# Kernel optimization log

Hardware: AMD Instinct MI355X
Metric: run time of the kernel (lower is better)

The kernel has to match this reference:

```python
import jax, jax.numpy as jnp
import numpy as np

N_NODES = 100000
N_EDGES = 1600000
DIM = 128
N_SEEDS = 15000


def _gcn_stack(edges, x, Ws):
    """Multi-layer GCN with sym-normalized edge-list aggregation, residual, ReLU.
    edges: [2, E] int; x: [N, d] float; Ws: list of [d, d] weights."""
    n = x.shape[0]
    loop = jnp.arange(n, dtype=edges.dtype)
    src = jnp.concatenate([edges[0], loop])  # add self-loops
    dst = jnp.concatenate([edges[1], loop])
    deg = jax.ops.segment_sum(jnp.ones(src.shape, x.dtype), dst, num_segments=n)
    dinv = jax.lax.rsqrt(deg)  # deg >= 1 thanks to self-loops
    norm = dinv[src] * dinv[dst]  # [E+N]
    for W in Ws:
        h = x @ W                                   # [N, d] dense transform
        msg = norm[:, None] * h[src]                # gather + scale, [E+N, d]
        agg = jax.ops.segment_sum(msg, dst, num_segments=n)  # scatter-add
        x = jax.nn.relu(agg + h)                    # residual + activation
    return x


def setup_inputs() -> dict:
    key = jax.random.key(0)
    ks = jax.random.split(key, 8)
    scale = 1.0 / np.sqrt(DIM)
    return {
        "sr_ent_seeds": jax.random.randint(ks[0], (N_SEEDS,), 0, N_NODES),
        "tg_ent_seeds": jax.random.randint(ks[1], (N_SEEDS,), 0, N_NODES),
        "edges_sr": jax.random.randint(ks[2], (2, N_EDGES), 0, N_NODES),
        "edges_tg": jax.random.randint(ks[3], (2, N_EDGES), 0, N_NODES),
        "embedding_sr": jax.random.normal(ks[4], (N_NODES, DIM), jnp.float32),
        "embedding_tg": jax.random.normal(ks[5], (N_NODES, DIM), jnp.float32),
        "W0": jax.random.normal(ks[6], (DIM, DIM), jnp.float32) * scale,
        "W1": jax.random.normal(ks[7], (DIM, DIM), jnp.float32) * scale,
    }


def reference(sr_ent_seeds, tg_ent_seeds, edges_sr, edges_tg,
              embedding_sr, embedding_tg, W0, W1):
    Ws = [W0, W1]
    sr_ent_hid = _gcn_stack(edges_sr, embedding_sr, Ws)
    tg_ent_hid = _gcn_stack(edges_tg, embedding_tg, Ws)
    sr_seed_hid = sr_ent_hid[sr_ent_seeds]
    tg_seed_hid = tg_ent_hid[tg_ent_seeds]
    return (sr_seed_hid, tg_seed_hid, sr_ent_hid, tg_ent_hid)
```

## Files before the change

kernel.cpp:

```cpp
#include <hip/hip_runtime.h>

#define NN 100000
#define NE 1600000
#define NT (2 * NN)
#define ET (2 * NE)
#define DIM 128
#define NS 15000
#define SB2 ((NT + 255) / 256)
#define PAD 136
#define NRANGE 16
#define RSZ (NT / NRANGE)
#define CH 16
#define BCAP 210000
#define NE4 (NE / 4)

typedef __attribute__((ext_vector_type(8))) short frag_ab;
typedef __attribute__((ext_vector_type(4))) float frag_cd;
typedef __attribute__((ext_vector_type(4))) int i4;

__device__ __forceinline__ unsigned short f2bf(float f) {
    unsigned int u = __float_as_uint(f);
    u += 0x7fff + ((u >> 16) & 1);
    return (unsigned short)(u >> 16);
}
__device__ __forceinline__ float bflo(unsigned int u) { return __uint_as_float(u << 16); }
__device__ __forceinline__ float bfhi(unsigned int u) { return __uint_as_float(u & 0xffff0000u); }

__global__ __launch_bounds__(256) void bucket_k(const int* __restrict__ e_sr,
                                                const int* __restrict__ e_tg,
                                                int* __restrict__ gcur,
                                                int* __restrict__ bkt) {
    __shared__ int bcnt[4][NRANGE];
    __shared__ int bbase[4][NRANGE];
    const int tid = threadIdx.x;
    if (tid < 4 * NRANGE) ((int*)bcnt)[tid] = 0;
    __syncthreads();
    const int g = blockIdx.x * 256 + tid;
    i4 s4, d4;
    if (g < NE4) {
        s4 = *((const i4*)e_sr + g);
        d4 = *((const i4*)e_sr + NE4 + g);
    } else {
        s4 = *((const i4*)e_tg + g - NE4);
        d4 = *((const i4*)e_tg + g);
        s4 += NN;
        d4 += NN;
    }
    const int wv = tid >> 6;
    int rr[4], lr[4];
#pragma unroll
    for (int j = 0; j < 4; ++j) {
        rr[j] = d4[j] / RSZ;
        lr[j] = atomicAdd(&bcnt[wv][rr[j]], 1);
    }
    __syncthreads();
    if (tid < NRANGE) {
        const int t0 = bcnt[0][tid], t1 = bcnt[1][tid];
        const int t2 = bcnt[2][tid], t3 = bcnt[3][tid];
        const int b = atomicAdd(&gcur[tid], t0 + t1 + t2 + t3);
        bbase[0][tid] = b;
        bbase[1][tid] = b + t0;
        bbase[2][tid] = b + t0 + t1;
        bbase[3][tid] = b + t0 + t1 + t2;
    }
    __syncthreads();
#pragma unroll
    for (int j = 0; j < 4; ++j) {
        const int dtl = d4[j] - rr[j] * RSZ;
        bkt[bbase[wv][rr[j]] + lr[j]] = (dtl << 18) | s4[j];
    }
}

__global__ __launch_bounds__(1024) void hist_k(const int* __restrict__ gcur,
                                               const int* __restrict__ bkt,
                                               int* __restrict__ P) {
    __shared__ int lc[RSZ];
    const int r = blockIdx.x & (NRANGE - 1);
    const int c = blockIdx.x >> 4;
    const int lo = r * RSZ;
    for (int i = threadIdx.x; i < RSZ; i += 1024) lc[i] = 0;
    __syncthreads();
    const int n_r = gcur[r] - r * BCAP;
    const int S = (n_r + CH - 1) / CH;
    const int s0 = c * S;
    int s1 = s0 + S; if (s1 > n_r) s1 = n_r;
    for (int v = s0 + threadIdx.x; v < s1; v += 1024) {
        const unsigned int w = (unsigned int)bkt[r * BCAP + v];
        atomicAdd(&lc[w >> 18], 1);
    }
    __syncthreads();
    for (int i = threadIdx.x; i < RSZ; i += 1024) P[c * NT + lo + i] = lc[i];
}

__global__ __launch_bounds__(256) void reduceA_k(const int* __restrict__ P,
                                                 int* __restrict__ cnt,
                                                 float* __restrict__ dinv,
                                                 int* __restrict__ bsum) {
    __shared__ int sh[256];
    const int t = threadIdx.x;
    const int i = blockIdx.x * 256 + t;
    int s = 0;
    if (i < NT) {
#pragma unroll
        for (int c = 0; c < CH; ++c) s += P[c * NT + i];
        cnt[i] = s;
        dinv[i] = rsqrtf((float)(s + 1));
    }
    sh[t] = s;
    __syncthreads();
    for (int off = 128; off > 0; off >>= 1) {
        if (t < off) sh[t] += sh[t + off];
        __syncthreads();
    }
    if (t == 0) bsum[blockIdx.x] = sh[0];
}

__global__ __launch_bounds__(1024) void scanB_k(int* bsum, int* row_ptr) {
    __shared__ int s[1024];
    const int t = threadIdx.x;
    const int v = (t < SB2) ? bsum[t] : 0;
    s[t] = v;
    __syncthreads();
    for (int off = 1; off < 1024; off <<= 1) {
        int add = (t >= off) ? s[t - off] : 0;
        __syncthreads();
        s[t] += add;
        __syncthreads();
    }
    if (t < SB2) bsum[t] = s[t] - v;
    if (t == SB2 - 1) row_ptr[NT] = s[t];
}

__global__ __launch_bounds__(256) void scanCbase_k(const int* __restrict__ cnt,
                                                   const int* __restrict__ bsum,
                                                   int* __restrict__ row_ptr,
                                                   int* __restrict__ P) {
    __shared__ int s[256];
    const int t = threadIdx.x;
    const int i = blockIdx.x * 256 + t;
    const int v = (i < NT) ? cnt[i] : 0;
    s[t] = v;
    __syncthreads();
    for (int off = 1; off < 256; off <<= 1) {
        int add = (t >= off) ? s[t - off] : 0;
        __syncthreads();
        s[t] += add;
        __syncthreads();
    }
    if (i < NT) {
        const int rp = bsum[blockIdx.x] + s[t] - v;
        row_ptr[i] = rp;
        int run = rp;
#pragma unroll
        for (int c = 0; c < CH; ++c) {
            const int pv = P[c * NT + i];
            P[c * NT + i] = run;
            run += pv;
        }
    }
}

__global__ __launch_bounds__(1024) void fillp_k(const int* __restrict__ gcur,
                                                const int* __restrict__ bkt,
                                                const int* __restrict__ P,
                                                int* __restrict__ csr_src) {
    __shared__ int cur[RSZ];
    const int r = blockIdx.x & (NRANGE - 1);
    const int c = blockIdx.x >> 4;
    const int lo = r * RSZ;
    for (int i = threadIdx.x; i < RSZ; i += 1024) cur[i] = P[c * NT + lo + i];
    __syncthreads();
    const int n_r = gcur[r] - r * BCAP;
    const int S = (n_r + CH - 1) / CH;
    const int s0 = c * S;
    int s1 = s0 + S; if (s1 > n_r) s1 = n_r;
    for (int v = s0 + threadIdx.x; v < s1; v += 1024) {
        const unsigned int w = (unsigned int)bkt[r * BCAP + v];
        const int pos = atomicAdd(&cur[w >> 18], 1);
        csr_src[pos] = (int)(w & 0x3FFFFu);
    }
}

__global__ __launch_bounds__(256) void convW2_k(const float* __restrict__ W0,
                                                const float* __restrict__ W1,
                                                unsigned short* __restrict__ wt0,
                                                unsigned short* __restrict__ wt1,
                                                int* __restrict__ gcur) {
    int i = blockIdx.x * 256 + threadIdx.x;
    if (blockIdx.x == 0 && threadIdx.x < NRANGE) gcur[threadIdx.x] = threadIdx.x * BCAP;
    if (i >= 2 * DIM * DIM) return;
    const float* W = (i < DIM * DIM) ? W0 : W1;
    unsigned short* wt = (i < DIM * DIM) ? wt0 : wt1;
    const int ii = i & (DIM * DIM - 1);
    const int n = ii & 127, k = ii >> 7;
    wt[n * DIM + k] = f2bf(W[k * DIM + n]);
}

__global__ __launch_bounds__(256) void gemmE_k(const float* __restrict__ emb_sr,
                                               const float* __restrict__ emb_tg,
                                               const unsigned short* __restrict__ Wt,
                                               const float* __restrict__ dinv,
                                               unsigned short* __restrict__ Gb) {
    __shared__ unsigned short xs[64 * PAD];
    __shared__ unsigned short ws[128 * PAD];
    const int tid = threadIdx.x;
    const int row0 = blockIdx.x * 64;

    for (int i = tid; i < 128 * 16; i += 256) {
        const int r = i >> 4, o = i & 15;
        *(uint4*)&ws[r * PAD + o * 8] = *(const uint4*)&Wt[r * DIM + o * 8];
    }
    for (int i = tid; i < 64 * 32; i += 256) {
        const int r = i >> 5, o = i & 31;
        const int gr = row0 + r;
        const float4 v = (gr < NN) ? ((const float4*)emb_sr)[gr * 32 + o]
                                   : ((const float4*)emb_tg)[(gr - NN) * 32 + o];
        ushort4 b;
        b.x = f2bf(v.x); b.y = f2bf(v.y); b.z = f2bf(v.z); b.w = f2bf(v.w);
        *(ushort4*)&xs[r * PAD + o * 4] = b;
    }
    __syncthreads();

    const int wave = tid >> 6;
    const int lane = tid & 63;
    const int m = lane & 15;
    const int quad = lane >> 4;
    const int rbase = wave * 16;

    frag_cd acc[8];
#pragma unroll
    for (int ct = 0; ct < 8; ct++) acc[ct] = (frag_cd){0.f, 0.f, 0.f, 0.f};

#pragma unroll
    for (int ks = 0; ks < 4; ks++) {
        const frag_ab a = *(const frag_ab*)&xs[(rbase + m) * PAD + ks * 32 + quad * 8];
#pragma unroll
        for (int ct = 0; ct < 8; ct++) {
            const frag_ab b = *(const frag_ab*)&ws[(ct * 16 + m) * PAD + ks * 32 + quad * 8];
            acc[ct] = __builtin_amdgcn_mfma_f32_16x16x32_bf16(a, b, acc[ct], 0, 0, 0);
        }
    }

#pragma unroll
    for (int r = 0; r < 4; r++) {
        const int grow = row0 + rbase + quad * 4 + r;
        const float dv = dinv[grow];
#pragma unroll
        for (int ct = 0; ct < 8; ct++)
            Gb[grow * DIM + ct * 16 + m] = f2bf(dv * acc[ct][r]);
    }
}

__global__ __launch_bounds__(256) void gemm_mfma_k(const unsigned short* __restrict__ Xb,
                                                   const unsigned short* __restrict__ Wt,
                                                   const float* __restrict__ dinv,
                                                   unsigned short* __restrict__ Gb) {
    __shared__ unsigned short xs[64 * PAD];
    __shared__ unsigned short ws[128 * PAD];
    const int tid = threadIdx.x;
    const int row0 = blockIdx.x * 64;

    for (int i = tid; i < 128 * 16; i += 256) {
        const int r = i >> 4, o = i & 15;
        *(uint4*)&ws[r * PAD + o * 8] = *(const uint4*)&Wt[r * DIM + o * 8];
    }
    for (int i = tid; i < 64 * 16; i += 256) {
        const int r = i >> 4, o = i & 15;
        *(uint4*)&xs[r * PAD + o * 8] = *(const uint4*)&Xb[(row0 + r) * DIM + o * 8];
    }
    __syncthreads();

    const int wave = tid >> 6;
    const int lane = tid & 63;
    const int m = lane & 15;
    const int quad = lane >> 4;
    const int rbase = wave * 16;

    frag_cd acc[8];
#pragma unroll
    for (int ct = 0; ct < 8; ct++) acc[ct] = (frag_cd){0.f, 0.f, 0.f, 0.f};

#pragma unroll
    for (int ks = 0; ks < 4; ks++) {
        const frag_ab a = *(const frag_ab*)&xs[(rbase + m) * PAD + ks * 32 + quad * 8];
#pragma unroll
        for (int ct = 0; ct < 8; ct++) {
            const frag_ab b = *(const frag_ab*)&ws[(ct * 16 + m) * PAD + ks * 32 + quad * 8];
            acc[ct] = __builtin_amdgcn_mfma_f32_16x16x32_bf16(a, b, acc[ct], 0, 0, 0);
        }
    }

#pragma unroll
    for (int r = 0; r < 4; r++) {
        const int grow = row0 + rbase + quad * 4 + r;
        const float dv = dinv[grow];
#pragma unroll
        for (int ct = 0; ct < 8; ct++)
            Gb[grow * DIM + ct * 16 + m] = f2bf(dv * acc[ct][r]);
    }
}

template <bool OUT_BF16>
__global__ __launch_bounds__(256) void pull_k(const int* __restrict__ row_ptr,
                                              const int* __restrict__ csr_src,
                                              const float* __restrict__ dinv,
                                              const unsigned short* __restrict__ Gb,
                                              float* __restrict__ outf,
                                              unsigned short* __restrict__ outb) {
    const int node = (blockIdx.x * 256 + threadIdx.x) >> 6;
    if (node >= NT) return;
    const int lane = threadIdx.x & 63;
    const unsigned int* __restrict__ G2 = (const unsigned int*)Gb;

    const int beg = row_ptr[node];
    const int end = row_ptr[node + 1];
    const float d = dinv[node];
    const float sq = 1.0f / d;

    const unsigned int gu = G2[node * 64 + lane];
    float sx = bflo(gu);
    float sy = bfhi(gu);
    const float hx = sx * sq;
    const float hy = sy * sq;

    for (int base = beg; base < end; base += 64) {
        int rem = end - base; if (rem > 64) rem = 64;
        const int sl = (lane < rem) ? csr_src[base + lane] : 0;
        int j = 0;
        for (; j + 16 <= rem; j += 16) {
            int ss[16];
            unsigned int mm[16];
#pragma unroll
            for (int q = 0; q < 16; ++q) ss[q] = __shfl(sl, j + q);
#pragma unroll
            for (int q = 0; q < 16; ++q) mm[q] = G2[ss[q] * 64 + lane];
#pragma unroll
            for (int q = 0; q < 16; ++q) { sx += bflo(mm[q]); sy += bfhi(mm[q]); }
        }
        for (; j + 8 <= rem; j += 8) {
            int ss[8];
            unsigned int mm[8];
#pragma unroll
            for (int q = 0; q < 8; ++q) ss[q] = __shfl(sl, j + q);
#pragma unroll
            for (int q = 0; q < 8; ++q) mm[q] = G2[ss[q] * 64 + lane];
#pragma unroll
            for (int q = 0; q < 8; ++q) { sx += bflo(mm[q]); sy += bfhi(mm[q]); }
        }
        for (; j + 4 <= rem; j += 4) {
            int ss[4];
            unsigned int mm[4];
#pragma unroll
            for (int q = 0; q < 4; ++q) ss[q] = __shfl(sl, j + q);
#pragma unroll
            for (int q = 0; q < 4; ++q) mm[q] = G2[ss[q] * 64 + lane];
#pragma unroll
            for (int q = 0; q < 4; ++q) { sx += bflo(mm[q]); sy += bfhi(mm[q]); }
        }
        for (; j < rem; ++j) {
            const int s = __shfl(sl, j);
            const unsigned int mu = G2[s * 64 + lane];
            sx += bflo(mu);
            sy += bfhi(mu);
        }
    }
    const float ax = fmaxf(d * sx + hx, 0.f);
    const float ay = fmaxf(d * sy + hy, 0.f);
    if (OUT_BF16) {
        ((unsigned int*)outb)[node * 64 + lane] =
            (unsigned int)f2bf(ax) | ((unsigned int)f2bf(ay) << 16);
    } else {
        float2 o; o.x = ax; o.y = ay;
        ((float2*)outf)[node * 64 + lane] = o;
    }
}

__global__ __launch_bounds__(256) void gather2_k(const int* __restrict__ sr_seeds,
                                                 const int* __restrict__ tg_seeds,
                                                 const float* __restrict__ ent,
                                                 float* __restrict__ sr_out,
                                                 float* __restrict__ tg_out) {
    const int gid = blockIdx.x * 256 + threadIdx.x;
    const int s = gid >> 5;
    if (s >= 2 * NS) return;
    const int q = gid & 31;
    const bool tg = s >= NS;
    const int si = tg ? s - NS : s;
    const int node = tg ? tg_seeds[si] + NN : sr_seeds[si];
    float* o = tg ? tg_out : sr_out;
    ((float4*)o)[si * 32 + q] = ((const float4*)ent)[node * 32 + q];
}

extern "C" void kernel_launch(void* const* d_in, const int* in_sizes, int n_in,
                              void* d_out, int out_size, void* d_ws, size_t ws_size,
                              hipStream_t stream) {
    const int* sr_seeds = (const int*)d_in[0];
    const int* tg_seeds = (const int*)d_in[1];
    const int* edges_sr = (const int*)d_in[2];
    const int* edges_tg = (const int*)d_in[3];
    const float* emb_sr = (const float*)d_in[4];
    const float* emb_tg = (const float*)d_in[5];
    const float* W0 = (const float*)d_in[6];
    const float* W1 = (const float*)d_in[7];
    float* out = (float*)d_out;

    int* cnt = (int*)d_ws;
    float* dinv = (float*)(cnt + 200704);
    int* row_ptr = (int*)(dinv + 200704);
    int* bsum = row_ptr + 200704;
    int* csr_src = bsum + 1024;
    unsigned short* wt0 = (unsigned short*)(csr_src + ET);
    unsigned short* wt1 = wt0 + DIM * DIM;
    unsigned short* hb = wt1 + DIM * DIM;
    int* P = (int*)hb;
    int* bkt = P + CH * NT;
    int* gcur = bsum + 800;

    float* sr_seed_out = out;
    float* tg_seed_out = out + (long long)NS * DIM;
    float* ent = out + (long long)2 * NS * DIM;
    unsigned short* xb = (unsigned short*)ent;

    const int gGemm = (NT + 63) / 64;
    const int gPull = NT / 4;
    const int gBkt = ET / 1024;
    const int gHF = NRANGE * CH;

    convW2_k<<<(2 * DIM * DIM + 255) / 256, 256, 0, stream>>>(W0, W1, wt0, wt1, gcur);

    bucket_k<<<gBkt, 256, 0, stream>>>(edges_sr, edges_tg, gcur, bkt);
    hist_k<<<gHF, 1024, 0, stream>>>(gcur, bkt, P);
    reduceA_k<<<SB2, 256, 0, stream>>>(P, cnt, dinv, bsum);
    scanB_k<<<1, 1024, 0, stream>>>(bsum, row_ptr);
    scanCbase_k<<<SB2, 256, 0, stream>>>(cnt, bsum, row_ptr, P);
    fillp_k<<<gHF, 1024, 0, stream>>>(gcur, bkt, P, csr_src);

    gemmE_k<<<gGemm, 256, 0, stream>>>(emb_sr, emb_tg, wt0, dinv, hb);
    pull_k<true><<<gPull, 256, 0, stream>>>(row_ptr, csr_src, dinv, hb, nullptr, xb);
    gemm_mfma_k<<<gGemm, 256, 0, stream>>>(xb, wt1, dinv, hb);
    pull_k<false><<<gPull, 256, 0, stream>>>(row_ptr, csr_src, dinv, hb, ent, nullptr);

    const int gSeed = (2 * NS * 32 + 255) / 256;
    gather2_k<<<gSeed, 256, 0, stream>>>(sr_seeds, tg_seeds, ent, sr_seed_out, tg_seed_out);
}
```

Measured before the change: 564.5 us.

## Split pull wave into half-waves, fuse block scan, read weights from global

The pull kernel now splits each 64-lane wave into two half-waves. Each lane loads 8-byte uint2 chunks, so two neighbour rows are gathered at once, and the halves are combined with a cross-lane xor shuffle. The single-block scanB kernel is removed: each scanCbase block reduces its preceding block sums itself, and the total is hardcoded to ET. The GEMM kernels stop staging weights in LDS and read B fragments directly from global memory. This cuts a launch and LDS traffic, at the cost of redundant prefix reads and uncached weight loads per block.

```diff
diff --git a/kernel.cpp b/kernel.cpp
--- a/kernel.cpp
+++ b/kernel.cpp
@@ -115,22 +115,6 @@
     if (t == 0) bsum[blockIdx.x] = sh[0];
 }
 
-__global__ __launch_bounds__(1024) void scanB_k(int* bsum, int* row_ptr) {
-    __shared__ int s[1024];
-    const int t = threadIdx.x;
-    const int v = (t < SB2) ? bsum[t] : 0;
-    s[t] = v;
-    __syncthreads();
-    for (int off = 1; off < 1024; off <<= 1) {
-        int add = (t >= off) ? s[t - off] : 0;
-        __syncthreads();
-        s[t] += add;
-        __syncthreads();
-    }
-    if (t < SB2) bsum[t] = s[t] - v;
-    if (t == SB2 - 1) row_ptr[NT] = s[t];
-}
-
 __global__ __launch_bounds__(256) void scanCbase_k(const int* __restrict__ cnt,
                                                    const int* __restrict__ bsum,
                                                    int* __restrict__ row_ptr,
@@ -138,6 +122,16 @@
     __shared__ int s[256];
     const int t = threadIdx.x;
     const int i = blockIdx.x * 256 + t;
+    int acc = 0;
+    for (int b = t; b < blockIdx.x; b += 256) acc += bsum[b];
+    s[t] = acc;
+    __syncthreads();
+    for (int off = 128; off > 0; off >>= 1) {
+        if (t < off) s[t] += s[t + off];
+        __syncthreads();
+    }
+    const int boff = s[0];
+    __syncthreads();
     const int v = (i < NT) ? cnt[i] : 0;
     s[t] = v;
     __syncthreads();
@@ -147,8 +141,9 @@
         s[t] += add;
         __syncthreads();
     }
+    if (blockIdx.x == 0 && t == 0) row_ptr[NT] = ET;
     if (i < NT) {
-        const int rp = bsum[blockIdx.x] + s[t] - v;
+        const int rp = boff + s[t] - v;
         row_ptr[i] = rp;
         int run = rp;
 #pragma unroll
@@ -202,14 +197,9 @@
                                                const float* __restrict__ dinv,
                                                unsigned short* __restrict__ Gb) {
     __shared__ unsigned short xs[64 * PAD];
-    __shared__ unsigned short ws[128 * PAD];
     const int tid = threadIdx.x;
     const int row0 = blockIdx.x * 64;
 
-    for (int i = tid; i < 128 * 16; i += 256) {
-        const int r = i >> 4, o = i & 15;
-        *(uint4*)&ws[r * PAD + o * 8] = *(const uint4*)&Wt[r * DIM + o * 8];
-    }
     for (int i = tid; i < 64 * 32; i += 256) {
         const int r = i >> 5, o = i & 31;
         const int gr = row0 + r;
@@ -236,7 +226,7 @@
         const frag_ab a = *(const frag_ab*)&xs[(rbase + m) * PAD + ks * 32 + quad * 8];
 #pragma unroll
         for (int ct = 0; ct < 8; ct++) {
-            const frag_ab b = *(const frag_ab*)&ws[(ct * 16 + m) * PAD + ks * 32 + quad * 8];
+            const frag_ab b = *(const frag_ab*)&Wt[(ct * 16 + m) * DIM + ks * 32 + quad * 8];
             acc[ct] = __builtin_amdgcn_mfma_f32_16x16x32_bf16(a, b, acc[ct], 0, 0, 0);
         }
     }
@@ -256,14 +246,9 @@
                                                    const float* __restrict__ dinv,
                                                    unsigned short* __restrict__ Gb) {
     __shared__ unsigned short xs[64 * PAD];
-    __shared__ unsigned short ws[128 * PAD];
     const int tid = threadIdx.x;
     const int row0 = blockIdx.x * 64;
 
-    for (int i = tid; i < 128 * 16; i += 256) {
-        const int r = i >> 4, o = i & 15;
-        *(uint4*)&ws[r * PAD + o * 8] = *(const uint4*)&Wt[r * DIM + o * 8];
-    }
     for (int i = tid; i < 64 * 16; i += 256) {
         const int r = i >> 4, o = i & 15;
         *(uint4*)&xs[r * PAD + o * 8] = *(const uint4*)&Xb[(row0 + r) * DIM + o * 8];
@@ -285,7 +270,7 @@
         const frag_ab a = *(const frag_ab*)&xs[(rbase + m) * PAD + ks * 32 + quad * 8];
 #pragma unroll
         for (int ct = 0; ct < 8; ct++) {
-            const frag_ab b = *(const frag_ab*)&ws[(ct * 16 + m) * PAD + ks * 32 + quad * 8];
+            const frag_ab b = *(const frag_ab*)&Wt[(ct * 16 + m) * DIM + ks * 32 + quad * 8];
             acc[ct] = __builtin_amdgcn_mfma_f32_16x16x32_bf16(a, b, acc[ct], 0, 0, 0);
         }
     }
@@ -310,68 +295,81 @@
     const int node = (blockIdx.x * 256 + threadIdx.x) >> 6;
     if (node >= NT) return;
     const int lane = threadIdx.x & 63;
-    const unsigned int* __restrict__ G2 = (const unsigned int*)Gb;
+    const int half = lane >> 5;
+    const int col = lane & 31;
+    const uint2* __restrict__ G4 = (const uint2*)Gb;
 
     const int beg = row_ptr[node];
     const int end = row_ptr[node + 1];
     const float d = dinv[node];
     const float sq = 1.0f / d;
 
-    const unsigned int gu = G2[node * 64 + lane];
-    float sx = bflo(gu);
-    float sy = bfhi(gu);
-    const float hx = sx * sq;
-    const float hy = sy * sq;
+    const uint2 su = G4[node * 32 + col];
+    float a0, a1, a2, a3;
+    if (half == 0) {
+        a0 = bflo(su.x); a1 = bfhi(su.x); a2 = bflo(su.y); a3 = bfhi(su.y);
+    } else {
+        a0 = a1 = a2 = a3 = 0.f;
+    }
 
     for (int base = beg; base < end; base += 64) {
         int rem = end - base; if (rem > 64) rem = 64;
         const int sl = (lane < rem) ? csr_src[base + lane] : 0;
         int j = 0;
         for (; j + 16 <= rem; j += 16) {
-            int ss[16];
-            unsigned int mm[16];
-#pragma unroll
-            for (int q = 0; q < 16; ++q) ss[q] = __shfl(sl, j + q);
-#pragma unroll
-            for (int q = 0; q < 16; ++q) mm[q] = G2[ss[q] * 64 + lane];
-#pragma unroll
-            for (int q = 0; q < 16; ++q) { sx += bflo(mm[q]); sy += bfhi(mm[q]); }
+            int ss[8]; uint2 mm[8];
+#pragma unroll
+            for (int q = 0; q < 8; ++q) ss[q] = __shfl(sl, j + 2 * q + half);
+#pragma unroll
+            for (int q = 0; q < 8; ++q) mm[q] = G4[ss[q] * 32 + col];
+#pragma unroll
+            for (int q = 0; q < 8; ++q) {
+                a0 += bflo(mm[q].x); a1 += bfhi(mm[q].x);
+                a2 += bflo(mm[q].y); a3 += bfhi(mm[q].y);
+            }
         }
         for (; j + 8 <= rem; j += 8) {
-            int ss[8];
-            unsigned int mm[8];
-#pragma unroll
-            for (int q = 0; q < 8; ++q) ss[q] = __shfl(sl, j + q);
-#pragma unroll
-            for (int q = 0; q < 8; ++q) mm[q] = G2[ss[q] * 64 + lane];
-#pragma unroll
-            for (int q = 0; q < 8; ++q) { sx += bflo(mm[q]); sy += bfhi(mm[q]); }
-        }
-        for (; j + 4 <= rem; j += 4) {
-            int ss[4];
-            unsigned int mm[4];
-#pragma unroll
-            for (int q = 0; q < 4; ++q) ss[q] = __shfl(sl, j + q);
-#pragma unroll
-            for (int q = 0; q < 4; ++q) mm[q] = G2[ss[q] * 64 + lane];
-#pragma unroll
-            for (int q = 0; q < 4; ++q) { sx += bflo(mm[q]); sy += bfhi(mm[q]); }
-        }
-        for (; j < rem; ++j) {
-            const int s = __shfl(sl, j);
-            const unsigned int mu = G2[s * 64 + lane];
-            sx += bflo(mu);
-            sy += bfhi(mu);
-        }
-    }
-    const float ax = fmaxf(d * sx + hx, 0.f);
-    const float ay = fmaxf(d * sy + hy, 0.f);
-    if (OUT_BF16) {
-        ((unsigned int*)outb)[node * 64 + lane] =
-            (unsigned int)f2bf(ax) | ((unsigned int)f2bf(ay) << 16);
-    } else {
-        float2 o; o.x = ax; o.y = ay;
-        ((float2*)outf)[node * 64 + lane] = o;
+            int ss[4]; uint2 mm[4];
+#pragma unroll
+            for (int q = 0; q < 4; ++q) ss[q] = __shfl(sl, j + 2 * q + half);
+#pragma unroll
+            for (int q = 0; q < 4; ++q) mm[q] = G4[ss[q] * 32 + col];
+#pragma unroll
+            for (int q = 0; q < 4; ++q) {
+                a0 += bflo(mm[q].x); a1 += bfhi(mm[q].x);
+                a2 += bflo(mm[q].y); a3 += bfhi(mm[q].y);
+            }
+        }
+        for (; j < rem; j += 2) {
+            const int j2 = j + half;
+            const int ssv = __shfl(sl, j2 & 63);
+            if (j2 < rem) {
+                const uint2 mu = G4[ssv * 32 + col];
+                a0 += bflo(mu.x); a1 += bfhi(mu.x);
+                a2 += bflo(mu.y); a3 += bfhi(mu.y);
+            }
+        }
+    }
+    a0 += __shfl_xor(a0, 32);
+    a1 += __shfl_xor(a1, 32);
+    a2 += __shfl_xor(a2, 32);
+    a3 += __shfl_xor(a3, 32);
+
+    const float r0 = fmaxf(d * a0 + bflo(su.x) * sq, 0.f);
+    const float r1 = fmaxf(d * a1 + bfhi(su.x) * sq, 0.f);
+    const float r2 = fmaxf(d * a2 + bflo(su.y) * sq, 0.f);
+    const float r3 = fmaxf(d * a3 + bfhi(su.y) * sq, 0.f);
+
+    if (half == 0) {
+        if (OUT_BF16) {
+            uint2 o;
+            o.x = (unsigned int)f2bf(r0) | ((unsigned int)f2bf(r1) << 16);
+            o.y = (unsigned int)f2bf(r2) | ((unsigned int)f2bf(r3) << 16);
+            ((uint2*)outb)[node * 32 + col] = o;
+        } else {
+            float4 o; o.x = r0; o.y = r1; o.z = r2; o.w = r3;
+            ((float4*)outf)[node * 32 + col] = o;
+        }
     }
 }
 
@@ -431,7 +429,6 @@
     bucket_k<<<gBkt, 256, 0, stream>>>(edges_sr, edges_tg, gcur, bkt);
     hist_k<<<gHF, 1024, 0, stream>>>(gcur, bkt, P);
     reduceA_k<<<SB2, 256, 0, stream>>>(P, cnt, dinv, bsum);
-    scanB_k<<<1, 1024, 0, stream>>>(bsum, row_ptr);
     scanCbase_k<<<SB2, 256, 0, stream>>>(cnt, bsum, row_ptr, P);
     fillp_k<<<gHF, 1024, 0, stream>>>(gcur, bkt, P, csr_src);
 
```

After: 628.2 us. 1.11x slower.
